# Performance work log

Measured on AMD Instinct MI355X. Metric: run time of the kernel, lower is better.

Reference implementation:

```python
import jax, jax.numpy as jnp
import numpy as np

WH = WW = 8          # window height/width
N_WIN = WH * WW      # tokens per window = 64
DIM = 256
NUM_HEADS = 8
CPB_HIDDEN = 512


def _rel_index():
    # Swin relative position index, shape (N, N), values in [0, (2Wh-1)*(2Ww-1))
    coords = np.stack(np.meshgrid(np.arange(WH), np.arange(WW), indexing='ij'))  # (2,Wh,Ww)
    flat = coords.reshape(2, -1)
    rel = (flat[:, :, None] - flat[:, None, :]).transpose(1, 2, 0)  # (N,N,2)
    rel[..., 0] += WH - 1
    rel[..., 1] += WW - 1
    rel[..., 0] *= 2 * WW - 1
    return rel.sum(-1).astype(np.int32)


def _coords_table():
    # normalized log-spaced continuous relative coordinates, shape (2Wh-1, 2Ww-1, 2)
    h = np.arange(-(WH - 1), WH, dtype=np.float32)
    w = np.arange(-(WW - 1), WW, dtype=np.float32)
    t = np.stack(np.meshgrid(h, w, indexing='ij'), axis=-1)
    t[..., 0] /= WH - 1
    t[..., 1] /= WW - 1
    t *= 8.0
    return (np.sign(t) * np.log2(np.abs(t) + 1.0) / np.log2(8.0)).astype(np.float32)


def setup_inputs() -> dict:
    key = jax.random.key(0)
    ks = jax.random.split(key, 6)
    B_ = 8192  # num_windows * batch
    x = jax.random.normal(ks[0], (B_, N_WIN, DIM), dtype=jnp.float32)
    qkv_weight = jax.random.normal(ks[1], (3 * DIM, DIM), dtype=jnp.float32) * 0.02
    q_bias = jnp.zeros((DIM,), dtype=jnp.float32)
    v_bias = jnp.zeros((DIM,), dtype=jnp.float32)
    logit_scale = jnp.log(10.0) * jnp.ones((NUM_HEADS, 1, 1), dtype=jnp.float32)
    cpb_w1 = jax.random.normal(ks[2], (CPB_HIDDEN, 2), dtype=jnp.float32) * 0.02
    cpb_b1 = jnp.zeros((CPB_HIDDEN,), dtype=jnp.float32)
    cpb_w2 = jax.random.normal(ks[3], (NUM_HEADS, CPB_HIDDEN), dtype=jnp.float32) * 0.02
    proj_w = jax.random.normal(ks[4], (DIM, DIM), dtype=jnp.float32) * 0.02
    proj_b = jnp.zeros((DIM,), dtype=jnp.float32)
    return {
        'x': x, 'qkv_weight': qkv_weight, 'q_bias': q_bias, 'v_bias': v_bias,
        'logit_scale': logit_scale, 'cpb_w1': cpb_w1, 'cpb_b1': cpb_b1,
        'cpb_w2': cpb_w2, 'proj_w': proj_w, 'proj_b': proj_b,
    }


def reference(x, qkv_weight, q_bias, v_bias, logit_scale, cpb_w1, cpb_b1, cpb_w2, proj_w, proj_b):
    B_, N, C = x.shape
    H = NUM_HEADS
    d = C // H
    # qkv projection: k-bias is fixed zero (Swin-V2 convention)
    qkv_b = jnp.concatenate([q_bias, jnp.zeros_like(v_bias), v_bias])
    qkv = x @ qkv_weight.T + qkv_b                       # (B_, N, 3C)
    qkv = qkv.reshape(B_, N, 3, H, d).transpose(2, 0, 3, 1, 4)  # (3, B_, H, N, d)
    q, k, v = qkv[0], qkv[1], qkv[2]
    # cosine attention (F.normalize with eps=1e-12)
    qn = q / jnp.maximum(jnp.linalg.norm(q, axis=-1, keepdims=True), 1e-12)
    kn = k / jnp.maximum(jnp.linalg.norm(k, axis=-1, keepdims=True), 1e-12)
    attn = jnp.einsum('bhnd,bhmd->bhnm', qn, kn)
    scale = jnp.exp(jnp.minimum(logit_scale, jnp.log(100.0)))  # clamp max = log(1/0.01)
    attn = attn * scale                                   # broadcasts (H,1,1)
    # continuous relative position bias via tiny MLP
    table = jnp.asarray(_coords_table())                  # (2Wh-1, 2Ww-1, 2)
    bias_table = jnp.maximum(table @ cpb_w1.T + cpb_b1, 0.0) @ cpb_w2.T  # (.., H)
    bias_table = bias_table.reshape(-1, H)
    idx = jnp.asarray(_rel_index().reshape(-1))
    bias = bias_table[idx].reshape(N, N, H).transpose(2, 0, 1)  # (H, N, N)
    attn = attn + 16.0 * jax.nn.sigmoid(bias)[None]
    attn = jax.nn.softmax(attn, axis=-1)
    out = jnp.einsum('bhnm,bhmd->bhnd', attn, v)          # (B_, H, N, d)
    out = out.transpose(0, 2, 1, 3).reshape(B_, N, C)
    return out @ proj_w.T + proj_b
```

## Files before the change

### kernel.cpp

```cpp
#include <hip/hip_runtime.h>
#include <hip/hip_fp16.h>

typedef _Float16 f16;
typedef _Float16 f16x8 __attribute__((ext_vector_type(8)));
typedef _Float16 f16x4 __attribute__((ext_vector_type(4)));
typedef float f32x4 __attribute__((ext_vector_type(4)));

#define L2E 1.4426950408889634f

#define WQ_OFF   0
#define PW_OFF   393216
#define QB_OFF   524288
#define SC_OFF   527360
#define TBL_OFF  527616
#define BB_OFF   535040


__global__ void prep0(const float* __restrict__ qw, const float* __restrict__ prw,
                      const float* __restrict__ qbias, const float* __restrict__ vbias,
                      const float* __restrict__ ls, char* __restrict__ ws) {
    int t = blockIdx.x * 256 + threadIdx.x;
    f16* wq = (f16*)(ws + WQ_OFF);
    f16* pw = (f16*)(ws + PW_OFF);
    if (t < 196608) wq[t] = (f16)qw[t];
    else            pw[t - 196608] = (f16)prw[t - 196608];
    if (t < 768) {
        float b = t < 256 ? qbias[t] : (t < 512 ? 0.f : vbias[t - 512]);
        ((float*)(ws + QB_OFF))[t] = b;
    }
    if (t < 8) ((float*)(ws + SC_OFF))[t] = expf(fminf(ls[t], 4.6051701859880914f));
}

__device__ __forceinline__ float norm_coord(int u) {
    float v = (float)(u - 7) * (8.0f / 7.0f);
    float s = (v > 0.f) ? 1.f : ((v < 0.f) ? -1.f : 0.f);
    return s * log2f(fabsf(v) + 1.f) * (1.f / 3.f);
}

__global__ void prep1(const float* __restrict__ w1, const float* __restrict__ b1,
                      const float* __restrict__ w2, char* __restrict__ ws) {
    int t = blockIdx.x * 256 + threadIdx.x;
    if (t >= 1800) return;
    int p = t >> 3, h = t & 7;
    float ta = norm_coord(p / 15);
    float tb = norm_coord(p % 15);
    float acc = 0.f;
    for (int j = 0; j < 512; ++j) {
        float hv = fmaf(w1[2 * j], ta, fmaf(w1[2 * j + 1], tb, b1[j]));
        acc = fmaf(fmaxf(hv, 0.f), w2[h * 512 + j], acc);
    }
    ((float*)(ws + TBL_OFF))[p * 8 + h] = acc;
}

__global__ void prep2(char* __restrict__ ws) {
    int t = blockIdx.x * 256 + threadIdx.x;
    int h = t >> 12, i = (t >> 6) & 63, j = t & 63;
    int ri = ((i >> 3) - (j >> 3) + 7) * 15 + ((i & 7) - (j & 7) + 7);
    float bv = ((const float*)(ws + TBL_OFF))[ri * 8 + h];
    float sg = 1.f / (1.f + expf(-bv));
    float sch = ((const float*)(ws + SC_OFF))[h];
    float val = (16.f * sg - sch - 16.f) * L2E + 14.0f;
    int mi = i >> 4, g = (i >> 2) & 3, r = i & 3;
    int nj = j >> 4, c = j & 15;
    int off = h * 4096 + mi * 1024 + nj * 256 + c * 16 + g * 4 + r;
    ((float*)(ws + BB_OFF))[off] = val;
}

#define SWZ(row) (((row) & 7) << 4)
#define LGKM0() asm volatile("s_waitcnt lgkmcnt(0)" ::: "memory")

__global__ __launch_bounds__(256, 2)
void swin_fused(const float* __restrict__ x, const f16* __restrict__ wq,
                const f16* __restrict__ pw, const float* __restrict__ qb,
                const float* __restrict__ sc, const float* __restrict__ bb2,
                const float* __restrict__ pb, float* __restrict__ out) {
    extern __shared__ char lds[];
    const int tid = threadIdx.x;
    const int lane = tid & 63;
    const int w = tid >> 6;
    const int g = lane >> 4;
    const int c = lane & 15;
    const int win = blockIdx.x;
    char* scr = lds + 32768 + w * 5120;

    const float* xw = x + (size_t)win * 16384;
    #pragma unroll
    for (int it = 0; it < 16; ++it) {
        int e4 = tid + it * 256;
        float4 v = ((const float4*)xw)[e4];
        int eidx = e4 * 4;
        int row = eidx >> 8, col = eidx & 255;
        f16x4 h4 = {(f16)v.x, (f16)v.y, (f16)v.z, (f16)v.w};
        int off = ((row << 9) + (col << 1)) ^ SWZ(row);
        *(f16x4*)(lds + off) = h4;
    }
    __syncthreads();

    f16x4 po[4][2];

    for (int hh = 0; hh < 2; ++hh) {
        const int h = w + hh * 4;

        f16x8 vf[2][2];
        {
            f32x4 acc[2][4] = {};
            #pragma unroll 2
            for (int kk = 0; kk < 8; ++kk) {
                int kb = kk * 32 + g * 8;
                f16x8 a[4];
                #pragma unroll
                for (int mi = 0; mi < 4; ++mi) {
                    int row = mi * 16 + c;
                    int off = ((row << 9) + (kb << 1)) ^ SWZ(row);
                    a[mi] = *(const f16x8*)(lds + off);
                }
                #pragma unroll
                for (int t = 0; t < 2; ++t) {
                    f16x8 b = *(const f16x8*)(wq + (size_t)(512 + h * 32 + t * 16 + c) * 256 + kb);
                    #pragma unroll
                    for (int mi = 0; mi < 4; ++mi)
                        acc[t][mi] = __builtin_amdgcn_mfma_f32_16x16x32_f16(a[mi], b, acc[t][mi], 0, 0, 0);
                }
            }
            #pragma unroll
            for (int t = 0; t < 2; ++t) {
                float bias = qb[512 + h * 32 + t * 16 + c];
                #pragma unroll
                for (int mi = 0; mi < 4; ++mi) {
                    f16x4 hv;
                    #pragma unroll
                    for (int r = 0; r < 4; ++r) hv[r] = (f16)(acc[t][mi][r] + bias);
                    int off = (t * 16 + c) * 144 + (mi * 16 + g * 4) * 2;
                    *(f16x4*)(scr + off) = hv;
                }
            }
        }
        LGKM0();
        #pragma unroll
        for (int dt = 0; dt < 2; ++dt)
            #pragma unroll
            for (int kt = 0; kt < 2; ++kt)
                vf[dt][kt] = *(const f16x8*)(scr + (dt * 16 + c) * 144 + kt * 64 + g * 16);
        LGKM0();

        f16x8 qf[4], kf[4];
        {
            f32x4 aq[2][4] = {};
            #pragma unroll 2
            for (int kk = 0; kk < 8; ++kk) {
                int kb = kk * 32 + g * 8;
                f16x8 a[4];
                #pragma unroll
                for (int mi = 0; mi < 4; ++mi) {
                    int row = mi * 16 + c;
                    int off = ((row << 9) + (kb << 1)) ^ SWZ(row);
                    a[mi] = *(const f16x8*)(lds + off);
                }
                #pragma unroll
                for (int t = 0; t < 2; ++t) {
                    f16x8 bq = *(const f16x8*)(wq + (size_t)(h * 32 + t * 16 + c) * 256 + kb);
                    #pragma unroll
                    for (int mi = 0; mi < 4; ++mi)
                        aq[t][mi] = __builtin_amdgcn_mfma_f32_16x16x32_f16(a[mi], bq, aq[t][mi], 0, 0, 0);
                }
            }
            #pragma unroll
            for (int t = 0; t < 2; ++t) {
                float bias = qb[h * 32 + t * 16 + c];
                #pragma unroll
                for (int mi = 0; mi < 4; ++mi)
                    #pragma unroll
                    for (int r = 0; r < 4; ++r) aq[t][mi][r] += bias;
            }
            #pragma unroll
            for (int mi = 0; mi < 4; ++mi) {
                #pragma unroll
                for (int r = 0; r < 4; ++r) {
                    float pq = aq[0][mi][r] * aq[0][mi][r] + aq[1][mi][r] * aq[1][mi][r];
                    pq += __shfl_xor(pq, 1); pq += __shfl_xor(pq, 2);
                    pq += __shfl_xor(pq, 4); pq += __shfl_xor(pq, 8);
                    float rq = __builtin_amdgcn_rsqf(fmaxf(pq, 1e-24f));
                    aq[0][mi][r] *= rq; aq[1][mi][r] *= rq;
                }
            }
            #pragma unroll
            for (int t = 0; t < 2; ++t)
                #pragma unroll
                for (int mi = 0; mi < 4; ++mi)
                    #pragma unroll
                    for (int r = 0; r < 4; ++r) {
                        int off = (mi * 16 + g * 4 + r) * 80 + (t * 16 + c) * 2;
                        *(f16*)(scr + off) = (f16)aq[t][mi][r];
                    }
            LGKM0();
            #pragma unroll
            for (int mi = 0; mi < 4; ++mi)
                qf[mi] = *(const f16x8*)(scr + (mi * 16 + c) * 80 + g * 16);
            LGKM0();
        }
        {
            f32x4 ak[2][4] = {};
            #pragma unroll 2
            for (int kk = 0; kk < 8; ++kk) {
                int kb = kk * 32 + g * 8;
                f16x8 a[4];
                #pragma unroll
                for (int mi = 0; mi < 4; ++mi) {
                    int row = mi * 16 + c;
                    int off = ((row << 9) + (kb << 1)) ^ SWZ(row);
                    a[mi] = *(const f16x8*)(lds + off);
                }
                #pragma unroll
                for (int t = 0; t < 2; ++t) {
                    f16x8 bk = *(const f16x8*)(wq + (size_t)(256 + h * 32 + t * 16 + c) * 256 + kb);
                    #pragma unroll
                    for (int mi = 0; mi < 4; ++mi)
                        ak[t][mi] = __builtin_amdgcn_mfma_f32_16x16x32_f16(a[mi], bk, ak[t][mi], 0, 0, 0);
                }
            }
            #pragma unroll
            for (int mi = 0; mi < 4; ++mi) {
                #pragma unroll
                for (int r = 0; r < 4; ++r) {
                    float pk = ak[0][mi][r] * ak[0][mi][r] + ak[1][mi][r] * ak[1][mi][r];
                    pk += __shfl_xor(pk, 1); pk += __shfl_xor(pk, 2);
                    pk += __shfl_xor(pk, 4); pk += __shfl_xor(pk, 8);
                    float rk = __builtin_amdgcn_rsqf(fmaxf(pk, 1e-24f));
                    ak[0][mi][r] *= rk; ak[1][mi][r] *= rk;
                }
            }
            #pragma unroll
            for (int t = 0; t < 2; ++t)
                #pragma unroll
                for (int mi = 0; mi < 4; ++mi)
                    #pragma unroll
                    for (int r = 0; r < 4; ++r) {
                        int off = (mi * 16 + g * 4 + r) * 80 + (t * 16 + c) * 2;
                        *(f16*)(scr + off) = (f16)ak[t][mi][r];
                    }
            LGKM0();
            #pragma unroll
            for (int nj = 0; nj < 4; ++nj)
                kf[nj] = *(const f16x8*)(scr + (nj * 16 + c) * 80 + g * 16);
            LGKM0();
        }

        if (hh == 1) {
            __syncthreads();
            const int h0 = w;
            #pragma unroll
            for (int mi = 0; mi < 4; ++mi)
                #pragma unroll
                for (int dt = 0; dt < 2; ++dt)
                    #pragma unroll
                    for (int r = 0; r < 4; ++r) {
                        int row = mi * 16 + g * 4 + r;
                        int col = h0 * 32 + dt * 16 + c;
                        int off = ((row << 9) + (col << 1)) ^ SWZ(row);
                        *(f16*)(lds + off) = po[mi][dt][r];
                    }
        }

        const float scl2e = sc[h] * L2E;
        const float* bbw = bb2 + h * 4096;
        f32x4 oo[4][2] = {};
        f32x4 oaux[4] = {};
        f16 onev = (c == 0) ? (f16)1.f : (f16)0.f;
        f16x8 von = {onev, onev, onev, onev, onev, onev, onev, onev};
        #pragma unroll
        for (int nj = 0; nj < 4; ++nj) {
            #pragma unroll
            for (int mi = 0; mi < 4; ++mi) {
                f32x4 z = {};
                f32x4 s = __builtin_amdgcn_mfma_f32_16x16x32_f16(qf[mi], kf[nj], z, 0, 0, 0);
                f32x4 bb4 = *(const f32x4*)(bbw + mi * 1024 + nj * 256 + c * 16 + g * 4);
                #pragma unroll
                for (int r = 0; r < 4; ++r) {
                    float e = exp2f(fmaf(s[r], scl2e, bb4[r]));
                    int off = (mi * 16 + g * 4 + r) * 80 + (((nj & 1) * 16 + c) << 1);
                    *(f16*)(scr + off) = (f16)e;
                }
            }
            if (nj & 1) {
                const int kt = nj >> 1;
                LGKM0();
                f16x8 pa[4];
                #pragma unroll
                for (int mo = 0; mo < 4; ++mo)
                    pa[mo] = *(const f16x8*)(scr + (mo * 16 + c) * 80 + g * 16);
                LGKM0();
                #pragma unroll
                for (int mo = 0; mo < 4; ++mo) {
                    #pragma unroll
                    for (int dt = 0; dt < 2; ++dt)
                        oo[mo][dt] = __builtin_amdgcn_mfma_f32_16x16x32_f16(pa[mo], vf[dt][kt], oo[mo][dt], 0, 0, 0);
                    oaux[mo] = __builtin_amdgcn_mfma_f32_16x16x32_f16(pa[mo], von, oaux[mo], 0, 0, 0);
                }
            }
        }
        #pragma unroll
        for (int mo = 0; mo < 4; ++mo)
            #pragma unroll
            for (int r = 0; r < 4; ++r) {
                float rsum = __shfl(oaux[mo][r], lane & 48);
                float ri = __builtin_amdgcn_rcpf(rsum);
                oo[mo][0][r] *= ri;
                oo[mo][1][r] *= ri;
            }
        if (hh == 0) {
            #pragma unroll
            for (int mi = 0; mi < 4; ++mi)
                #pragma unroll
                for (int dt = 0; dt < 2; ++dt)
                    #pragma unroll
                    for (int r = 0; r < 4; ++r)
                        po[mi][dt][r] = (f16)oo[mi][dt][r];
        } else {
            #pragma unroll
            for (int mi = 0; mi < 4; ++mi)
                #pragma unroll
                for (int dt = 0; dt < 2; ++dt)
                    #pragma unroll
                    for (int r = 0; r < 4; ++r) {
                        int row = mi * 16 + g * 4 + r;
                        int col = h * 32 + dt * 16 + c;
                        int off = ((row << 9) + (col << 1)) ^ SWZ(row);
                        *(f16*)(lds + off) = (f16)oo[mi][dt][r];
                    }
        }
    }
    __syncthreads();

    float pbias[4];
    #pragma unroll
    for (int nt = 0; nt < 4; ++nt) pbias[nt] = pb[w * 64 + nt * 16 + c];
    f32x4 pacc[4][4] = {};
    #pragma unroll 2
    for (int kk = 0; kk < 8; ++kk) {
        int kb = kk * 32 + g * 8;
        f16x8 a[4];
        #pragma unroll
        for (int mi = 0; mi < 4; ++mi) {
            int row = mi * 16 + c;
            int off = ((row << 9) + (kb << 1)) ^ SWZ(row);
            a[mi] = *(const f16x8*)(lds + off);
        }
        #pragma unroll
        for (int nt = 0; nt < 4; ++nt) {
            f16x8 b = *(const f16x8*)(pw + (size_t)(w * 64 + nt * 16 + c) * 256 + kb);
            #pragma unroll
            for (int mi = 0; mi < 4; ++mi)
                pacc[nt][mi] = __builtin_amdgcn_mfma_f32_16x16x32_f16(a[mi], b, pacc[nt][mi], 0, 0, 0);
        }
    }
    __syncthreads();

    #pragma unroll
    for (int p = 0; p < 2; ++p) {
        #pragma unroll
        for (int nt = 0; nt < 4; ++nt)
            #pragma unroll
            for (int m2 = 0; m2 < 2; ++m2) {
                int mi = p * 2 + m2;
                #pragma unroll
                for (int r = 0; r < 4; ++r) {
                    int row = m2 * 16 + g * 4 + r;
                    int col = w * 64 + nt * 16 + c;
                    int off = (row * 1024 + col * 4) ^ ((row & 7) << 4);
                    *(float*)(lds + off) = pacc[nt][mi][r] + pbias[nt];
                }
            }
        __syncthreads();
        float4* out4 = (float4*)(out + (size_t)win * 16384 + p * 8192);
        #pragma unroll
        for (int it = 0; it < 8; ++it) {
            int e4 = it * 256 + tid;
            int off = (e4 * 16) ^ (((e4 >> 6) & 7) << 4);
            out4[e4] = *(const float4*)(lds + off);
        }
        if (p == 0) __syncthreads();
    }
}


extern "C" void kernel_launch(void* const* d_in, const int* in_sizes, int n_in,
                              void* d_out, int out_size, void* d_ws, size_t ws_size,
                              hipStream_t stream) {
    (void)in_sizes; (void)n_in; (void)out_size; (void)ws_size;
    const float* x   = (const float*)d_in[0];
    const float* qw  = (const float*)d_in[1];
    const float* qb_ = (const float*)d_in[2];
    const float* vb_ = (const float*)d_in[3];
    const float* ls  = (const float*)d_in[4];
    const float* w1  = (const float*)d_in[5];
    const float* b1  = (const float*)d_in[6];
    const float* w2  = (const float*)d_in[7];
    const float* prw = (const float*)d_in[8];
    const float* pb  = (const float*)d_in[9];
    float* out = (float*)d_out;
    char* ws = (char*)d_ws;

    prep0<<<1024, 256, 0, stream>>>(qw, prw, qb_, vb_, ls, ws);
    prep1<<<8, 256, 0, stream>>>(w1, b1, w2, ws);
    prep2<<<128, 256, 0, stream>>>(ws);

    (void)hipFuncSetAttribute((const void*)swin_fused,
                              hipFuncAttributeMaxDynamicSharedMemorySize, 53248);
    swin_fused<<<8192, 256, 53248, stream>>>(
        x,
        (const f16*)(ws + WQ_OFF), (const f16*)(ws + PW_OFF),
        (const float*)(ws + QB_OFF), (const float*)(ws + SC_OFF),
        (const float*)(ws + BB_OFF), pb, out);
}
```

Baseline: 772.0 us.

## Raise occupancy to 3 blocks/CU by cutting registers in softmax sum and projection

```diff
diff --git a/kernel.cpp b/kernel.cpp
--- a/kernel.cpp
+++ b/kernel.cpp
@@ -69,7 +69,7 @@
 #define SWZ(row) (((row) & 7) << 4)
 #define LGKM0() asm volatile("s_waitcnt lgkmcnt(0)" ::: "memory")
 
-__global__ __launch_bounds__(256, 2)
+__global__ __launch_bounds__(256, 3)
 void swin_fused(const float* __restrict__ x, const f16* __restrict__ wq,
                 const f16* __restrict__ pw, const float* __restrict__ qb,
                 const float* __restrict__ sc, const float* __restrict__ bb2,
@@ -82,6 +82,7 @@
     const int c = lane & 15;
     const int win = blockIdx.x;
     char* scr = lds + 32768 + w * 5120;
+    char* stg = lds + 32768;
 
     const float* xw = x + (size_t)win * 16384;
     #pragma unroll
@@ -264,9 +265,7 @@
         const float scl2e = sc[h] * L2E;
         const float* bbw = bb2 + h * 4096;
         f32x4 oo[4][2] = {};
-        f32x4 oaux[4] = {};
-        f16 onev = (c == 0) ? (f16)1.f : (f16)0.f;
-        f16x8 von = {onev, onev, onev, onev, onev, onev, onev, onev};
+        f32x4 rs[4] = {};
         #pragma unroll
         for (int nj = 0; nj < 4; ++nj) {
             #pragma unroll
@@ -277,6 +276,7 @@
                 #pragma unroll
                 for (int r = 0; r < 4; ++r) {
                     float e = exp2f(fmaf(s[r], scl2e, bb4[r]));
+                    rs[mi][r] += e;
                     int off = (mi * 16 + g * 4 + r) * 80 + (((nj & 1) * 16 + c) << 1);
                     *(f16*)(scr + off) = (f16)e;
                 }
@@ -290,22 +290,22 @@
                     pa[mo] = *(const f16x8*)(scr + (mo * 16 + c) * 80 + g * 16);
                 LGKM0();
                 #pragma unroll
-                for (int mo = 0; mo < 4; ++mo) {
+                for (int mo = 0; mo < 4; ++mo)
                     #pragma unroll
                     for (int dt = 0; dt < 2; ++dt)
                         oo[mo][dt] = __builtin_amdgcn_mfma_f32_16x16x32_f16(pa[mo], vf[dt][kt], oo[mo][dt], 0, 0, 0);
-                    oaux[mo] = __builtin_amdgcn_mfma_f32_16x16x32_f16(pa[mo], von, oaux[mo], 0, 0, 0);
-                }
             }
         }
         #pragma unroll
-        for (int mo = 0; mo < 4; ++mo)
+        for (int mi = 0; mi < 4; ++mi)
             #pragma unroll
             for (int r = 0; r < 4; ++r) {
-                float rsum = __shfl(oaux[mo][r], lane & 48);
-                float ri = __builtin_amdgcn_rcpf(rsum);
-                oo[mo][0][r] *= ri;
-                oo[mo][1][r] *= ri;
+                float t = rs[mi][r];
+                t += __shfl_xor(t, 1); t += __shfl_xor(t, 2);
+                t += __shfl_xor(t, 4); t += __shfl_xor(t, 8);
+                float ri = __builtin_amdgcn_rcpf(t);
+                oo[mi][0][r] *= ri;
+                oo[mi][1][r] *= ri;
             }
         if (hh == 0) {
             #pragma unroll
@@ -334,51 +334,38 @@
     float pbias[4];
     #pragma unroll
     for (int nt = 0; nt < 4; ++nt) pbias[nt] = pb[w * 64 + nt * 16 + c];
-    f32x4 pacc[4][4] = {};
-    #pragma unroll 2
-    for (int kk = 0; kk < 8; ++kk) {
-        int kb = kk * 32 + g * 8;
-        f16x8 a[4];
-        #pragma unroll
-        for (int mi = 0; mi < 4; ++mi) {
-            int row = mi * 16 + c;
+    for (int cc = 0; cc < 4; ++cc) {
+        f32x4 pacc[4] = {};
+        #pragma unroll 2
+        for (int kk = 0; kk < 8; ++kk) {
+            int kb = kk * 32 + g * 8;
+            int row = cc * 16 + c;
             int off = ((row << 9) + (kb << 1)) ^ SWZ(row);
-            a[mi] = *(const f16x8*)(lds + off);
-        }
-        #pragma unroll
-        for (int nt = 0; nt < 4; ++nt) {
-            f16x8 b = *(const f16x8*)(pw + (size_t)(w * 64 + nt * 16 + c) * 256 + kb);
-            #pragma unroll
-            for (int mi = 0; mi < 4; ++mi)
-                pacc[nt][mi] = __builtin_amdgcn_mfma_f32_16x16x32_f16(a[mi], b, pacc[nt][mi], 0, 0, 0);
-        }
-    }
-    __syncthreads();
-
-    #pragma unroll
-    for (int p = 0; p < 2; ++p) {
+            f16x8 a = *(const f16x8*)(lds + off);
+            #pragma unroll
+            for (int nt = 0; nt < 4; ++nt) {
+                f16x8 b = *(const f16x8*)(pw + (size_t)(w * 64 + nt * 16 + c) * 256 + kb);
+                pacc[nt] = __builtin_amdgcn_mfma_f32_16x16x32_f16(a, b, pacc[nt], 0, 0, 0);
+            }
+        }
+        __syncthreads();
         #pragma unroll
         for (int nt = 0; nt < 4; ++nt)
             #pragma unroll
-            for (int m2 = 0; m2 < 2; ++m2) {
-                int mi = p * 2 + m2;
-                #pragma unroll
-                for (int r = 0; r < 4; ++r) {
-                    int row = m2 * 16 + g * 4 + r;
-                    int col = w * 64 + nt * 16 + c;
-                    int off = (row * 1024 + col * 4) ^ ((row & 7) << 4);
-                    *(float*)(lds + off) = pacc[nt][mi][r] + pbias[nt];
-                }
+            for (int r = 0; r < 4; ++r) {
+                int row = g * 4 + r;
+                int col = w * 64 + nt * 16 + c;
+                int off = (row * 1024 + col * 4) ^ ((row & 7) << 4);
+                *(float*)(stg + off) = pacc[nt][r] + pbias[nt];
             }
         __syncthreads();
-        float4* out4 = (float4*)(out + (size_t)win * 16384 + p * 8192);
+        float4* out4 = (float4*)(out + (size_t)win * 16384 + cc * 4096);
         #pragma unroll
-        for (int it = 0; it < 8; ++it) {
+        for (int it = 0; it < 4; ++it) {
             int e4 = it * 256 + tid;
             int off = (e4 * 16) ^ (((e4 >> 6) & 7) << 4);
-            out4[e4] = *(const float4*)(lds + off);
-        }
-        if (p == 0) __syncthreads();
+            out4[e4] = *(const float4*)(stg + off);
+        }
     }
 }
 
```

After: 1.260 ms. +63.2%, slower.

## Replace LDS round-trips for Q/K/V fragments with register shuffles and transposed MFMAs

Applied to the files above, without the earlier changes.

```diff
diff --git a/kernel.cpp b/kernel.cpp
--- a/kernel.cpp
+++ b/kernel.cpp
@@ -64,6 +64,27 @@
     int nj = j >> 4, c = j & 15;
     int off = h * 4096 + mi * 1024 + nj * 256 + c * 16 + g * 4 + r;
     ((float*)(ws + BB_OFF))[off] = val;
+}
+
+__device__ __forceinline__ void packh4(f32x4 v, unsigned &lo, unsigned &hi) {
+    union { f16x4 h; unsigned u[2]; } t;
+    t.h[0] = (f16)v[0]; t.h[1] = (f16)v[1]; t.h[2] = (f16)v[2]; t.h[3] = (f16)v[3];
+    lo = t.u[0]; hi = t.u[1];
+}
+__device__ __forceinline__ f16x8 xchg4(unsigned p0l, unsigned p0h,
+                                       unsigned p1l, unsigned p1h,
+                                       int g, int c) {
+    int sLo = ((g & 1) << 5) + c;
+    int sHi = sLo + 16;
+    unsigned a0 = (unsigned)__shfl((int)p0l, sLo), a1 = (unsigned)__shfl((int)p0h, sLo);
+    unsigned b0 = (unsigned)__shfl((int)p1l, sLo), b1 = (unsigned)__shfl((int)p1h, sLo);
+    unsigned c0 = (unsigned)__shfl((int)p0l, sHi), c1 = (unsigned)__shfl((int)p0h, sHi);
+    unsigned d0 = (unsigned)__shfl((int)p1l, sHi), d1 = (unsigned)__shfl((int)p1h, sHi);
+    bool up = g >= 2;
+    union { f16x8 h; unsigned u[4]; } r;
+    r.u[0] = up ? b0 : a0; r.u[1] = up ? b1 : a1;
+    r.u[2] = up ? d0 : c0; r.u[3] = up ? d1 : c1;
+    return r.h;
 }
 
 #define SWZ(row) (((row) & 7) << 4)
@@ -100,10 +121,10 @@
 
     for (int hh = 0; hh < 2; ++hh) {
         const int h = w + hh * 4;
-
-        f16x8 vf[2][2];
+        f16x8 vf[2][2], qf[4], kf[4];
+
         {
-            f32x4 acc[2][4] = {};
+            f32x4 av[2][4] = {};
             #pragma unroll 2
             for (int kk = 0; kk < 8; ++kk) {
                 int kb = kk * 32 + g * 8;
@@ -119,31 +140,31 @@
                     f16x8 b = *(const f16x8*)(wq + (size_t)(512 + h * 32 + t * 16 + c) * 256 + kb);
                     #pragma unroll
                     for (int mi = 0; mi < 4; ++mi)
-                        acc[t][mi] = __builtin_amdgcn_mfma_f32_16x16x32_f16(a[mi], b, acc[t][mi], 0, 0, 0);
+                        av[t][mi] = __builtin_amdgcn_mfma_f32_16x16x32_f16(a[mi], b, av[t][mi], 0, 0, 0);
                 }
             }
             #pragma unroll
             for (int t = 0; t < 2; ++t) {
                 float bias = qb[512 + h * 32 + t * 16 + c];
                 #pragma unroll
-                for (int mi = 0; mi < 4; ++mi) {
-                    f16x4 hv;
-                    #pragma unroll
-                    for (int r = 0; r < 4; ++r) hv[r] = (f16)(acc[t][mi][r] + bias);
-                    int off = (t * 16 + c) * 144 + (mi * 16 + g * 4) * 2;
-                    *(f16x4*)(scr + off) = hv;
-                }
-            }
-        }
-        LGKM0();
-        #pragma unroll
-        for (int dt = 0; dt < 2; ++dt)
-            #pragma unroll
-            for (int kt = 0; kt < 2; ++kt)
-                vf[dt][kt] = *(const f16x8*)(scr + (dt * 16 + c) * 144 + kt * 64 + g * 16);
-        LGKM0();
-
-        f16x8 qf[4], kf[4];
+                for (int mi = 0; mi < 4; ++mi)
+                    #pragma unroll
+                    for (int r = 0; r < 4; ++r) av[t][mi][r] += bias;
+            }
+            unsigned pv[2][4][2];
+            #pragma unroll
+            for (int t = 0; t < 2; ++t)
+                #pragma unroll
+                for (int mi = 0; mi < 4; ++mi)
+                    packh4(av[t][mi], pv[t][mi][0], pv[t][mi][1]);
+            #pragma unroll
+            for (int dt = 0; dt < 2; ++dt)
+                #pragma unroll
+                for (int kt = 0; kt < 2; ++kt)
+                    vf[dt][kt] = xchg4(pv[dt][2 * kt][0], pv[dt][2 * kt][1],
+                                       pv[dt][2 * kt + 1][0], pv[dt][2 * kt + 1][1], g, c);
+        }
+
         {
             f32x4 aq[2][4] = {};
             #pragma unroll 2
@@ -151,52 +172,48 @@
                 int kb = kk * 32 + g * 8;
                 f16x8 a[4];
                 #pragma unroll
-                for (int mi = 0; mi < 4; ++mi) {
-                    int row = mi * 16 + c;
+                for (int nt = 0; nt < 4; ++nt) {
+                    int row = nt * 16 + c;
                     int off = ((row << 9) + (kb << 1)) ^ SWZ(row);
-                    a[mi] = *(const f16x8*)(lds + off);
-                }
-                #pragma unroll
-                for (int t = 0; t < 2; ++t) {
-                    f16x8 bq = *(const f16x8*)(wq + (size_t)(h * 32 + t * 16 + c) * 256 + kb);
-                    #pragma unroll
-                    for (int mi = 0; mi < 4; ++mi)
-                        aq[t][mi] = __builtin_amdgcn_mfma_f32_16x16x32_f16(a[mi], bq, aq[t][mi], 0, 0, 0);
-                }
-            }
-            #pragma unroll
-            for (int t = 0; t < 2; ++t) {
-                float bias = qb[h * 32 + t * 16 + c];
-                #pragma unroll
-                for (int mi = 0; mi < 4; ++mi)
-                    #pragma unroll
-                    for (int r = 0; r < 4; ++r) aq[t][mi][r] += bias;
-            }
-            #pragma unroll
-            for (int mi = 0; mi < 4; ++mi) {
-                #pragma unroll
-                for (int r = 0; r < 4; ++r) {
-                    float pq = aq[0][mi][r] * aq[0][mi][r] + aq[1][mi][r] * aq[1][mi][r];
-                    pq += __shfl_xor(pq, 1); pq += __shfl_xor(pq, 2);
-                    pq += __shfl_xor(pq, 4); pq += __shfl_xor(pq, 8);
-                    float rq = __builtin_amdgcn_rsqf(fmaxf(pq, 1e-24f));
-                    aq[0][mi][r] *= rq; aq[1][mi][r] *= rq;
-                }
-            }
-            #pragma unroll
-            for (int t = 0; t < 2; ++t)
-                #pragma unroll
-                for (int mi = 0; mi < 4; ++mi)
-                    #pragma unroll
-                    for (int r = 0; r < 4; ++r) {
-                        int off = (mi * 16 + g * 4 + r) * 80 + (t * 16 + c) * 2;
-                        *(f16*)(scr + off) = (f16)aq[t][mi][r];
-                    }
-            LGKM0();
-            #pragma unroll
-            for (int mi = 0; mi < 4; ++mi)
-                qf[mi] = *(const f16x8*)(scr + (mi * 16 + c) * 80 + g * 16);
-            LGKM0();
+                    a[nt] = *(const f16x8*)(lds + off);
+                }
+                #pragma unroll
+                for (int mt = 0; mt < 2; ++mt) {
+                    f16x8 bq = *(const f16x8*)(wq + (size_t)(h * 32 + mt * 16 + c) * 256 + kb);
+                    #pragma unroll
+                    for (int nt = 0; nt < 4; ++nt)
+                        aq[mt][nt] = __builtin_amdgcn_mfma_f32_16x16x32_f16(bq, a[nt], aq[mt][nt], 0, 0, 0);
+                }
+            }
+            f32x4 qb4[2];
+            #pragma unroll
+            for (int mt = 0; mt < 2; ++mt)
+                qb4[mt] = *(const f32x4*)(qb + h * 32 + mt * 16 + g * 4);
+            #pragma unroll
+            for (int mt = 0; mt < 2; ++mt)
+                #pragma unroll
+                for (int nt = 0; nt < 4; ++nt)
+                    aq[mt][nt] += qb4[mt];
+            #pragma unroll
+            for (int nt = 0; nt < 4; ++nt) {
+                float pq = 0.f;
+                #pragma unroll
+                for (int mt = 0; mt < 2; ++mt)
+                    #pragma unroll
+                    for (int r = 0; r < 4; ++r) pq = fmaf(aq[mt][nt][r], aq[mt][nt][r], pq);
+                pq += __shfl_xor(pq, 16);
+                pq += __shfl_xor(pq, 32);
+                float rq = __builtin_amdgcn_rsqf(fmaxf(pq, 1e-24f));
+                #pragma unroll
+                for (int mt = 0; mt < 2; ++mt) aq[mt][nt] *= rq;
+            }
+            #pragma unroll
+            for (int nt = 0; nt < 4; ++nt) {
+                unsigned q0l, q0h, q1l, q1h;
+                packh4(aq[0][nt], q0l, q0h);
+                packh4(aq[1][nt], q1l, q1h);
+                qf[nt] = xchg4(q0l, q0h, q1l, q1h, g, c);
+            }
         }
         {
             f32x4 ak[2][4] = {};
@@ -205,44 +222,39 @@
                 int kb = kk * 32 + g * 8;
                 f16x8 a[4];
                 #pragma unroll
-                for (int mi = 0; mi < 4; ++mi) {
-                    int row = mi * 16 + c;
+                for (int nt = 0; nt < 4; ++nt) {
+                    int row = nt * 16 + c;
                     int off = ((row << 9) + (kb << 1)) ^ SWZ(row);
-                    a[mi] = *(const f16x8*)(lds + off);
-                }
-                #pragma unroll
-                for (int t = 0; t < 2; ++t) {
-                    f16x8 bk = *(const f16x8*)(wq + (size_t)(256 + h * 32 + t * 16 + c) * 256 + kb);
-                    #pragma unroll
-                    for (int mi = 0; mi < 4; ++mi)
-                        ak[t][mi] = __builtin_amdgcn_mfma_f32_16x16x32_f16(a[mi], bk, ak[t][mi], 0, 0, 0);
-                }
-            }
-            #pragma unroll
-            for (int mi = 0; mi < 4; ++mi) {
-                #pragma unroll
-                for (int r = 0; r < 4; ++r) {
-                    float pk = ak[0][mi][r] * ak[0][mi][r] + ak[1][mi][r] * ak[1][mi][r];
-                    pk += __shfl_xor(pk, 1); pk += __shfl_xor(pk, 2);
-                    pk += __shfl_xor(pk, 4); pk += __shfl_xor(pk, 8);
-                    float rk = __builtin_amdgcn_rsqf(fmaxf(pk, 1e-24f));
-                    ak[0][mi][r] *= rk; ak[1][mi][r] *= rk;
-                }
-            }
-            #pragma unroll
-            for (int t = 0; t < 2; ++t)
-                #pragma unroll
-                for (int mi = 0; mi < 4; ++mi)
-                    #pragma unroll
-                    for (int r = 0; r < 4; ++r) {
-                        int off = (mi * 16 + g * 4 + r) * 80 + (t * 16 + c) * 2;
-                        *(f16*)(scr + off) = (f16)ak[t][mi][r];
-                    }
-            LGKM0();
-            #pragma unroll
-            for (int nj = 0; nj < 4; ++nj)
-                kf[nj] = *(const f16x8*)(scr + (nj * 16 + c) * 80 + g * 16);
-            LGKM0();
+                    a[nt] = *(const f16x8*)(lds + off);
+                }
+                #pragma unroll
+                for (int mt = 0; mt < 2; ++mt) {
+                    f16x8 bk = *(const f16x8*)(wq + (size_t)(256 + h * 32 + mt * 16 + c) * 256 + kb);
+                    #pragma unroll
+                    for (int nt = 0; nt < 4; ++nt)
+                        ak[mt][nt] = __builtin_amdgcn_mfma_f32_16x16x32_f16(bk, a[nt], ak[mt][nt], 0, 0, 0);
+                }
+            }
+            #pragma unroll
+            for (int nt = 0; nt < 4; ++nt) {
+                float pk = 0.f;
+                #pragma unroll
+                for (int mt = 0; mt < 2; ++mt)
+                    #pragma unroll
+                    for (int r = 0; r < 4; ++r) pk = fmaf(ak[mt][nt][r], ak[mt][nt][r], pk);
+                pk += __shfl_xor(pk, 16);
+                pk += __shfl_xor(pk, 32);
+                float rk = __builtin_amdgcn_rsqf(fmaxf(pk, 1e-24f));
+                #pragma unroll
+                for (int mt = 0; mt < 2; ++mt) ak[mt][nt] *= rk;
+            }
+            #pragma unroll
+            for (int nt = 0; nt < 4; ++nt) {
+                unsigned k0l, k0h, k1l, k1h;
+                packh4(ak[0][nt], k0l, k0h);
+                packh4(ak[1][nt], k1l, k1h);
+                kf[nt] = xchg4(k0l, k0h, k1l, k1h, g, c);
+            }
         }
 
         if (hh == 1) {
@@ -264,9 +276,7 @@
         const float scl2e = sc[h] * L2E;
         const float* bbw = bb2 + h * 4096;
         f32x4 oo[4][2] = {};
-        f32x4 oaux[4] = {};
-        f16 onev = (c == 0) ? (f16)1.f : (f16)0.f;
-        f16x8 von = {onev, onev, onev, onev, onev, onev, onev, onev};
+        f32x4 rs[4] = {};
         #pragma unroll
         for (int nj = 0; nj < 4; ++nj) {
             #pragma unroll
@@ -277,6 +287,7 @@
                 #pragma unroll
                 for (int r = 0; r < 4; ++r) {
                     float e = exp2f(fmaf(s[r], scl2e, bb4[r]));
+                    rs[mi][r] += e;
                     int off = (mi * 16 + g * 4 + r) * 80 + (((nj & 1) * 16 + c) << 1);
                     *(f16*)(scr + off) = (f16)e;
                 }
@@ -290,22 +301,22 @@
                     pa[mo] = *(const f16x8*)(scr + (mo * 16 + c) * 80 + g * 16);
                 LGKM0();
                 #pragma unroll
-                for (int mo = 0; mo < 4; ++mo) {
+                for (int mo = 0; mo < 4; ++mo)
                     #pragma unroll
                     for (int dt = 0; dt < 2; ++dt)
                         oo[mo][dt] = __builtin_amdgcn_mfma_f32_16x16x32_f16(pa[mo], vf[dt][kt], oo[mo][dt], 0, 0, 0);
-                    oaux[mo] = __builtin_amdgcn_mfma_f32_16x16x32_f16(pa[mo], von, oaux[mo], 0, 0, 0);
-                }
-            }
-        }
-        #pragma unroll
-        for (int mo = 0; mo < 4; ++mo)
+            }
+        }
+        #pragma unroll
+        for (int mi = 0; mi < 4; ++mi)
             #pragma unroll
             for (int r = 0; r < 4; ++r) {
-                float rsum = __shfl(oaux[mo][r], lane & 48);
-                float ri = __builtin_amdgcn_rcpf(rsum);
-                oo[mo][0][r] *= ri;
-                oo[mo][1][r] *= ri;
+                float t = rs[mi][r];
+                t += __shfl_xor(t, 1); t += __shfl_xor(t, 2);
+                t += __shfl_xor(t, 4); t += __shfl_xor(t, 8);
+                float ri = __builtin_amdgcn_rcpf(t);
+                oo[mi][0][r] *= ri;
+                oo[mi][1][r] *= ri;
             }
         if (hh == 0) {
             #pragma unroll
```

Result: slower. 984.9 us (+27.6%).

## Make fused Swin kernel persistent with register prefetch of next window

Applied to the files above, without the earlier changes.

```diff
diff --git a/kernel.cpp b/kernel.cpp
--- a/kernel.cpp
+++ b/kernel.cpp
@@ -80,305 +80,330 @@
     const int w = tid >> 6;
     const int g = lane >> 4;
     const int c = lane & 15;
-    const int win = blockIdx.x;
     char* scr = lds + 32768 + w * 5120;
 
-    const float* xw = x + (size_t)win * 16384;
-    #pragma unroll
+    float4 pf[16];
+
     for (int it = 0; it < 16; ++it) {
-        int e4 = tid + it * 256;
-        float4 v = ((const float4*)xw)[e4];
-        int eidx = e4 * 4;
-        int row = eidx >> 8, col = eidx & 255;
-        f16x4 h4 = {(f16)v.x, (f16)v.y, (f16)v.z, (f16)v.w};
-        int off = ((row << 9) + (col << 1)) ^ SWZ(row);
-        *(f16x4*)(lds + off) = h4;
-    }
-    __syncthreads();
-
-    f16x4 po[4][2];
-
-    for (int hh = 0; hh < 2; ++hh) {
-        const int h = w + hh * 4;
-
-        f16x8 vf[2][2];
-        {
-            f32x4 acc[2][4] = {};
-            #pragma unroll 2
-            for (int kk = 0; kk < 8; ++kk) {
-                int kb = kk * 32 + g * 8;
-                f16x8 a[4];
+        const int win = blockIdx.x + it * 512;
+
+        if (it == 0) {
+            const float* xw = x + (size_t)win * 16384;
+            #pragma unroll
+            for (int q = 0; q < 16; ++q) {
+                int e4 = tid + q * 256;
+                float4 v = ((const float4*)xw)[e4];
+                int eidx = e4 * 4;
+                int row = eidx >> 8, col = eidx & 255;
+                f16x4 h4 = {(f16)v.x, (f16)v.y, (f16)v.z, (f16)v.w};
+                int off = ((row << 9) + (col << 1)) ^ SWZ(row);
+                *(f16x4*)(lds + off) = h4;
+            }
+        } else {
+            #pragma unroll
+            for (int q = 0; q < 16; ++q) {
+                int e4 = tid + q * 256;
+                int eidx = e4 * 4;
+                int row = eidx >> 8, col = eidx & 255;
+                f16x4 h4 = {(f16)pf[q].x, (f16)pf[q].y, (f16)pf[q].z, (f16)pf[q].w};
+                int off = ((row << 9) + (col << 1)) ^ SWZ(row);
+                *(f16x4*)(lds + off) = h4;
+            }
+        }
+        __syncthreads();
+
+        f16x4 po[4][2];
+
+        for (int hh = 0; hh < 2; ++hh) {
+            const int h = w + hh * 4;
+
+            f16x8 vf[2][2];
+            {
+                f32x4 acc[2][4] = {};
+                #pragma unroll 2
+                for (int kk = 0; kk < 8; ++kk) {
+                    int kb = kk * 32 + g * 8;
+                    f16x8 a[4];
+                    #pragma unroll
+                    for (int mi = 0; mi < 4; ++mi) {
+                        int row = mi * 16 + c;
+                        int off = ((row << 9) + (kb << 1)) ^ SWZ(row);
+                        a[mi] = *(const f16x8*)(lds + off);
+                    }
+                    #pragma unroll
+                    for (int t = 0; t < 2; ++t) {
+                        f16x8 b = *(const f16x8*)(wq + (size_t)(512 + h * 32 + t * 16 + c) * 256 + kb);
+                        #pragma unroll
+                        for (int mi = 0; mi < 4; ++mi)
+                            acc[t][mi] = __builtin_amdgcn_mfma_f32_16x16x32_f16(a[mi], b, acc[t][mi], 0, 0, 0);
+                    }
+                }
+                #pragma unroll
+                for (int t = 0; t < 2; ++t) {
+                    float bias = qb[512 + h * 32 + t * 16 + c];
+                    #pragma unroll
+                    for (int mi = 0; mi < 4; ++mi) {
+                        f16x4 hv;
+                        #pragma unroll
+                        for (int r = 0; r < 4; ++r) hv[r] = (f16)(acc[t][mi][r] + bias);
+                        int off = (t * 16 + c) * 144 + (mi * 16 + g * 4) * 2;
+                        *(f16x4*)(scr + off) = hv;
+                    }
+                }
+            }
+            LGKM0();
+            #pragma unroll
+            for (int dt = 0; dt < 2; ++dt)
+                #pragma unroll
+                for (int kt = 0; kt < 2; ++kt)
+                    vf[dt][kt] = *(const f16x8*)(scr + (dt * 16 + c) * 144 + kt * 64 + g * 16);
+            LGKM0();
+
+            f16x8 qf[4], kf[4];
+            {
+                f32x4 aq[2][4] = {};
+                #pragma unroll 2
+                for (int kk = 0; kk < 8; ++kk) {
+                    int kb = kk * 32 + g * 8;
+                    f16x8 a[4];
+                    #pragma unroll
+                    for (int mi = 0; mi < 4; ++mi) {
+                        int row = mi * 16 + c;
+                        int off = ((row << 9) + (kb << 1)) ^ SWZ(row);
+                        a[mi] = *(const f16x8*)(lds + off);
+                    }
+                    #pragma unroll
+                    for (int t = 0; t < 2; ++t) {
+                        f16x8 bq = *(const f16x8*)(wq + (size_t)(h * 32 + t * 16 + c) * 256 + kb);
+                        #pragma unroll
+                        for (int mi = 0; mi < 4; ++mi)
+                            aq[t][mi] = __builtin_amdgcn_mfma_f32_16x16x32_f16(a[mi], bq, aq[t][mi], 0, 0, 0);
+                    }
+                }
+                #pragma unroll
+                for (int t = 0; t < 2; ++t) {
+                    float bias = qb[h * 32 + t * 16 + c];
+                    #pragma unroll
+                    for (int mi = 0; mi < 4; ++mi)
+                        #pragma unroll
+                        for (int r = 0; r < 4; ++r) aq[t][mi][r] += bias;
+                }
                 #pragma unroll
                 for (int mi = 0; mi < 4; ++mi) {
-                    int row = mi * 16 + c;
-                    int off = ((row << 9) + (kb << 1)) ^ SWZ(row);
-                    a[mi] = *(const f16x8*)(lds + off);
-                }
-                #pragma unroll
-                for (int t = 0; t < 2; ++t) {
-                    f16x8 b = *(const f16x8*)(wq + (size_t)(512 + h * 32 + t * 16 + c) * 256 + kb);
+                    #pragma unroll
+                    for (int r = 0; r < 4; ++r) {
+                        float pq = aq[0][mi][r] * aq[0][mi][r] + aq[1][mi][r] * aq[1][mi][r];
+                        pq += __shfl_xor(pq, 1); pq += __shfl_xor(pq, 2);
+                        pq += __shfl_xor(pq, 4); pq += __shfl_xor(pq, 8);
+                        float rq = __builtin_amdgcn_rsqf(fmaxf(pq, 1e-24f));
+                        aq[0][mi][r] *= rq; aq[1][mi][r] *= rq;
+                    }
+                }
+                #pragma unroll
+                for (int t = 0; t < 2; ++t)
                     #pragma unroll
                     for (int mi = 0; mi < 4; ++mi)
-                        acc[t][mi] = __builtin_amdgcn_mfma_f32_16x16x32_f16(a[mi], b, acc[t][mi], 0, 0, 0);
-                }
-            }
-            #pragma unroll
-            for (int t = 0; t < 2; ++t) {
-                float bias = qb[512 + h * 32 + t * 16 + c];
+                        #pragma unroll
+                        for (int r = 0; r < 4; ++r) {
+                            int off = (mi * 16 + g * 4 + r) * 80 + (t * 16 + c) * 2;
+                            *(f16*)(scr + off) = (f16)aq[t][mi][r];
+                        }
+                LGKM0();
+                #pragma unroll
+                for (int mi = 0; mi < 4; ++mi)
+                    qf[mi] = *(const f16x8*)(scr + (mi * 16 + c) * 80 + g * 16);
+                LGKM0();
+            }
+            {
+                f32x4 ak[2][4] = {};
+                #pragma unroll 2
+                for (int kk = 0; kk < 8; ++kk) {
+                    int kb = kk * 32 + g * 8;
+                    f16x8 a[4];
+                    #pragma unroll
+                    for (int mi = 0; mi < 4; ++mi) {
+                        int row = mi * 16 + c;
+                        int off = ((row << 9) + (kb << 1)) ^ SWZ(row);
+                        a[mi] = *(const f16x8*)(lds + off);
+                    }
+                    #pragma unroll
+                    for (int t = 0; t < 2; ++t) {
+                        f16x8 bk = *(const f16x8*)(wq + (size_t)(256 + h * 32 + t * 16 + c) * 256 + kb);
+                        #pragma unroll
+                        for (int mi = 0; mi < 4; ++mi)
+                            ak[t][mi] = __builtin_amdgcn_mfma_f32_16x16x32_f16(a[mi], bk, ak[t][mi], 0, 0, 0);
+                    }
+                }
                 #pragma unroll
                 for (int mi = 0; mi < 4; ++mi) {
-                    f16x4 hv;
-                    #pragma unroll
-                    for (int r = 0; r < 4; ++r) hv[r] = (f16)(acc[t][mi][r] + bias);
-                    int off = (t * 16 + c) * 144 + (mi * 16 + g * 4) * 2;
-                    *(f16x4*)(scr + off) = hv;
-                }
+                    #pragma unroll
+                    for (int r = 0; r < 4; ++r) {
+                        float pk = ak[0][mi][r] * ak[0][mi][r] + ak[1][mi][r] * ak[1][mi][r];
+                        pk += __shfl_xor(pk, 1); pk += __shfl_xor(pk, 2);
+                        pk += __shfl_xor(pk, 4); pk += __shfl_xor(pk, 8);
+                        float rk = __builtin_amdgcn_rsqf(fmaxf(pk, 1e-24f));
+                        ak[0][mi][r] *= rk; ak[1][mi][r] *= rk;
+                    }
+                }
+                #pragma unroll
+                for (int t = 0; t < 2; ++t)
+                    #pragma unroll
+                    for (int mi = 0; mi < 4; ++mi)
+                        #pragma unroll
+                        for (int r = 0; r < 4; ++r) {
+                            int off = (mi * 16 + g * 4 + r) * 80 + (t * 16 + c) * 2;
+                            *(f16*)(scr + off) = (f16)ak[t][mi][r];
+                        }
+                LGKM0();
+                #pragma unroll
+                for (int nj = 0; nj < 4; ++nj)
+                    kf[nj] = *(const f16x8*)(scr + (nj * 16 + c) * 80 + g * 16);
+                LGKM0();
+            }
+
+            if (hh == 1) {
+                __syncthreads();
+                const int h0 = w;
+                #pragma unroll
+                for (int mi = 0; mi < 4; ++mi)
+                    #pragma unroll
+                    for (int dt = 0; dt < 2; ++dt)
+                        #pragma unroll
+                        for (int r = 0; r < 4; ++r) {
+                            int row = mi * 16 + g * 4 + r;
+                            int col = h0 * 32 + dt * 16 + c;
+                            int off = ((row << 9) + (col << 1)) ^ SWZ(row);
+                            *(f16*)(lds + off) = po[mi][dt][r];
+                        }
+            }
+
+            const float scl2e = sc[h] * L2E;
+            const float* bbw = bb2 + h * 4096;
+            f32x4 oo[4][2] = {};
+            f32x4 oaux[4] = {};
+            f16 onev = (c == 0) ? (f16)1.f : (f16)0.f;
+            f16x8 von = {onev, onev, onev, onev, onev, onev, onev, onev};
+            #pragma unroll
+            for (int nj = 0; nj < 4; ++nj) {
+                #pragma unroll
+                for (int mi = 0; mi < 4; ++mi) {
+                    f32x4 z = {};
+                    f32x4 s = __builtin_amdgcn_mfma_f32_16x16x32_f16(qf[mi], kf[nj], z, 0, 0, 0);
+                    f32x4 bb4 = *(const f32x4*)(bbw + mi * 1024 + nj * 256 + c * 16 + g * 4);
+                    #pragma unroll
+                    for (int r = 0; r < 4; ++r) {
+                        float e = exp2f(fmaf(s[r], scl2e, bb4[r]));
+                        int off = (mi * 16 + g * 4 + r) * 80 + (((nj & 1) * 16 + c) << 1);
+                        *(f16*)(scr + off) = (f16)e;
+                    }
+                }
+                if (nj & 1) {
+                    const int kt = nj >> 1;
+                    LGKM0();
+                    f16x8 pa[4];
+                    #pragma unroll
+                    for (int mo = 0; mo < 4; ++mo)
+                        pa[mo] = *(const f16x8*)(scr + (mo * 16 + c) * 80 + g * 16);
+                    LGKM0();
+                    #pragma unroll
+                    for (int mo = 0; mo < 4; ++mo) {
+                        #pragma unroll
+                        for (int dt = 0; dt < 2; ++dt)
+                            oo[mo][dt] = __builtin_amdgcn_mfma_f32_16x16x32_f16(pa[mo], vf[dt][kt], oo[mo][dt], 0, 0, 0);
+                        oaux[mo] = __builtin_amdgcn_mfma_f32_16x16x32_f16(pa[mo], von, oaux[mo], 0, 0, 0);
+                    }
+                }
+            }
+            #pragma unroll
+            for (int mo = 0; mo < 4; ++mo)
+                #pragma unroll
+                for (int r = 0; r < 4; ++r) {
+                    float rsum = __shfl(oaux[mo][r], lane & 48);
+                    float ri = __builtin_amdgcn_rcpf(rsum);
+                    oo[mo][0][r] *= ri;
+                    oo[mo][1][r] *= ri;
+                }
+            if (hh == 0) {
+                #pragma unroll
+                for (int mi = 0; mi < 4; ++mi)
+                    #pragma unroll
+                    for (int dt = 0; dt < 2; ++dt)
+                        #pragma unroll
+                        for (int r = 0; r < 4; ++r)
+                            po[mi][dt][r] = (f16)oo[mi][dt][r];
+            } else {
+                #pragma unroll
+                for (int mi = 0; mi < 4; ++mi)
+                    #pragma unroll
+                    for (int dt = 0; dt < 2; ++dt)
+                        #pragma unroll
+                        for (int r = 0; r < 4; ++r) {
+                            int row = mi * 16 + g * 4 + r;
+                            int col = h * 32 + dt * 16 + c;
+                            int off = ((row << 9) + (col << 1)) ^ SWZ(row);
+                            *(f16*)(lds + off) = (f16)oo[mi][dt][r];
+                        }
             }
         }
-        LGKM0();
+        __syncthreads();
+
+        if (it < 15) {
+            const float* xn = x + (size_t)(win + 512) * 16384;
+            #pragma unroll
+            for (int q = 0; q < 16; ++q)
+                pf[q] = ((const float4*)xn)[tid + q * 256];
+        }
+
+        float pbias[4];
         #pragma unroll
-        for (int dt = 0; dt < 2; ++dt)
-            #pragma unroll
-            for (int kt = 0; kt < 2; ++kt)
-                vf[dt][kt] = *(const f16x8*)(scr + (dt * 16 + c) * 144 + kt * 64 + g * 16);
-        LGKM0();
-
-        f16x8 qf[4], kf[4];
-        {
-            f32x4 aq[2][4] = {};
-            #pragma unroll 2
-            for (int kk = 0; kk < 8; ++kk) {
-                int kb = kk * 32 + g * 8;
-                f16x8 a[4];
-                #pragma unroll
-                for (int mi = 0; mi < 4; ++mi) {
-                    int row = mi * 16 + c;
-                    int off = ((row << 9) + (kb << 1)) ^ SWZ(row);
-                    a[mi] = *(const f16x8*)(lds + off);
-                }
-                #pragma unroll
-                for (int t = 0; t < 2; ++t) {
-                    f16x8 bq = *(const f16x8*)(wq + (size_t)(h * 32 + t * 16 + c) * 256 + kb);
-                    #pragma unroll
-                    for (int mi = 0; mi < 4; ++mi)
-                        aq[t][mi] = __builtin_amdgcn_mfma_f32_16x16x32_f16(a[mi], bq, aq[t][mi], 0, 0, 0);
-                }
-            }
-            #pragma unroll
-            for (int t = 0; t < 2; ++t) {
-                float bias = qb[h * 32 + t * 16 + c];
+        for (int nt = 0; nt < 4; ++nt) pbias[nt] = pb[w * 64 + nt * 16 + c];
+        f32x4 pacc[4][4] = {};
+        #pragma unroll 2
+        for (int kk = 0; kk < 8; ++kk) {
+            int kb = kk * 32 + g * 8;
+            f16x8 a[4];
+            #pragma unroll
+            for (int mi = 0; mi < 4; ++mi) {
+                int row = mi * 16 + c;
+                int off = ((row << 9) + (kb << 1)) ^ SWZ(row);
+                a[mi] = *(const f16x8*)(lds + off);
+            }
+            #pragma unroll
+            for (int nt = 0; nt < 4; ++nt) {
+                f16x8 b = *(const f16x8*)(pw + (size_t)(w * 64 + nt * 16 + c) * 256 + kb);
                 #pragma unroll
                 for (int mi = 0; mi < 4; ++mi)
-                    #pragma unroll
-                    for (int r = 0; r < 4; ++r) aq[t][mi][r] += bias;
-            }
-            #pragma unroll
-            for (int mi = 0; mi < 4; ++mi) {
-                #pragma unroll
-                for (int r = 0; r < 4; ++r) {
-                    float pq = aq[0][mi][r] * aq[0][mi][r] + aq[1][mi][r] * aq[1][mi][r];
-                    pq += __shfl_xor(pq, 1); pq += __shfl_xor(pq, 2);
-                    pq += __shfl_xor(pq, 4); pq += __shfl_xor(pq, 8);
-                    float rq = __builtin_amdgcn_rsqf(fmaxf(pq, 1e-24f));
-                    aq[0][mi][r] *= rq; aq[1][mi][r] *= rq;
-                }
-            }
-            #pragma unroll
-            for (int t = 0; t < 2; ++t)
-                #pragma unroll
-                for (int mi = 0; mi < 4; ++mi)
+                    pacc[nt][mi] = __builtin_amdgcn_mfma_f32_16x16x32_f16(a[mi], b, pacc[nt][mi], 0, 0, 0);
+            }
+        }
+        __syncthreads();
+
+        #pragma unroll
+        for (int p = 0; p < 2; ++p) {
+            #pragma unroll
+            for (int nt = 0; nt < 4; ++nt)
+                #pragma unroll
+                for (int m2 = 0; m2 < 2; ++m2) {
+                    int mi = p * 2 + m2;
                     #pragma unroll
                     for (int r = 0; r < 4; ++r) {
-                        int off = (mi * 16 + g * 4 + r) * 80 + (t * 16 + c) * 2;
-                        *(f16*)(scr + off) = (f16)aq[t][mi][r];
-                    }
-            LGKM0();
-            #pragma unroll
-            for (int mi = 0; mi < 4; ++mi)
-                qf[mi] = *(const f16x8*)(scr + (mi * 16 + c) * 80 + g * 16);
-            LGKM0();
+                        int row = m2 * 16 + g * 4 + r;
+                        int col = w * 64 + nt * 16 + c;
+                        int off = (row * 1024 + col * 4) ^ ((row & 7) << 4);
+                        *(float*)(lds + off) = pacc[nt][mi][r] + pbias[nt];
+                    }
+                }
+            __syncthreads();
+            float4* out4 = (float4*)(out + (size_t)win * 16384 + p * 8192);
+            #pragma unroll
+            for (int q = 0; q < 8; ++q) {
+                int e4 = q * 256 + tid;
+                int off = (e4 * 16) ^ (((e4 >> 6) & 7) << 4);
+                out4[e4] = *(const float4*)(lds + off);
+            }
+            if (p == 0) __syncthreads();
         }
-        {
-            f32x4 ak[2][4] = {};
-            #pragma unroll 2
-            for (int kk = 0; kk < 8; ++kk) {
-                int kb = kk * 32 + g * 8;
-                f16x8 a[4];
-                #pragma unroll
-                for (int mi = 0; mi < 4; ++mi) {
-                    int row = mi * 16 + c;
-                    int off = ((row << 9) + (kb << 1)) ^ SWZ(row);
-                    a[mi] = *(const f16x8*)(lds + off);
-                }
-                #pragma unroll
-                for (int t = 0; t < 2; ++t) {
-                    f16x8 bk = *(const f16x8*)(wq + (size_t)(256 + h * 32 + t * 16 + c) * 256 + kb);
-                    #pragma unroll
-                    for (int mi = 0; mi < 4; ++mi)
-                        ak[t][mi] = __builtin_amdgcn_mfma_f32_16x16x32_f16(a[mi], bk, ak[t][mi], 0, 0, 0);
-                }
-            }
-            #pragma unroll
-            for (int mi = 0; mi < 4; ++mi) {
-                #pragma unroll
-                for (int r = 0; r < 4; ++r) {
-                    float pk = ak[0][mi][r] * ak[0][mi][r] + ak[1][mi][r] * ak[1][mi][r];
-                    pk += __shfl_xor(pk, 1); pk += __shfl_xor(pk, 2);
-                    pk += __shfl_xor(pk, 4); pk += __shfl_xor(pk, 8);
-                    float rk = __builtin_amdgcn_rsqf(fmaxf(pk, 1e-24f));
-                    ak[0][mi][r] *= rk; ak[1][mi][r] *= rk;
-                }
-            }
-            #pragma unroll
-            for (int t = 0; t < 2; ++t)
-                #pragma unroll
-                for (int mi = 0; mi < 4; ++mi)
-                    #pragma unroll
-                    for (int r = 0; r < 4; ++r) {
-                        int off = (mi * 16 + g * 4 + r) * 80 + (t * 16 + c) * 2;
-                        *(f16*)(scr + off) = (f16)ak[t][mi][r];
-                    }
-            LGKM0();
-            #pragma unroll
-            for (int nj = 0; nj < 4; ++nj)
-                kf[nj] = *(const f16x8*)(scr + (nj * 16 + c) * 80 + g * 16);
-            LGKM0();
-        }
-
-        if (hh == 1) {
-            __syncthreads();
-            const int h0 = w;
-            #pragma unroll
-            for (int mi = 0; mi < 4; ++mi)
-                #pragma unroll
-                for (int dt = 0; dt < 2; ++dt)
-                    #pragma unroll
-                    for (int r = 0; r < 4; ++r) {
-                        int row = mi * 16 + g * 4 + r;
-                        int col = h0 * 32 + dt * 16 + c;
-                        int off = ((row << 9) + (col << 1)) ^ SWZ(row);
-                        *(f16*)(lds + off) = po[mi][dt][r];
-                    }
-        }
-
-        const float scl2e = sc[h] * L2E;
-        const float* bbw = bb2 + h * 4096;
-        f32x4 oo[4][2] = {};
-        f32x4 oaux[4] = {};
-        f16 onev = (c == 0) ? (f16)1.f : (f16)0.f;
-        f16x8 von = {onev, onev, onev, onev, onev, onev, onev, onev};
-        #pragma unroll
-        for (int nj = 0; nj < 4; ++nj) {
-            #pragma unroll
-            for (int mi = 0; mi < 4; ++mi) {
-                f32x4 z = {};
-                f32x4 s = __builtin_amdgcn_mfma_f32_16x16x32_f16(qf[mi], kf[nj], z, 0, 0, 0);
-                f32x4 bb4 = *(const f32x4*)(bbw + mi * 1024 + nj * 256 + c * 16 + g * 4);
-                #pragma unroll
-                for (int r = 0; r < 4; ++r) {
-                    float e = exp2f(fmaf(s[r], scl2e, bb4[r]));
-                    int off = (mi * 16 + g * 4 + r) * 80 + (((nj & 1) * 16 + c) << 1);
-                    *(f16*)(scr + off) = (f16)e;
-                }
-            }
-            if (nj & 1) {
-                const int kt = nj >> 1;
-                LGKM0();
-                f16x8 pa[4];
-                #pragma unroll
-                for (int mo = 0; mo < 4; ++mo)
-                    pa[mo] = *(const f16x8*)(scr + (mo * 16 + c) * 80 + g * 16);
-                LGKM0();
-                #pragma unroll
-                for (int mo = 0; mo < 4; ++mo) {
-                    #pragma unroll
-                    for (int dt = 0; dt < 2; ++dt)
-                        oo[mo][dt] = __builtin_amdgcn_mfma_f32_16x16x32_f16(pa[mo], vf[dt][kt], oo[mo][dt], 0, 0, 0);
-                    oaux[mo] = __builtin_amdgcn_mfma_f32_16x16x32_f16(pa[mo], von, oaux[mo], 0, 0, 0);
-                }
-            }
-        }
-        #pragma unroll
-        for (int mo = 0; mo < 4; ++mo)
-            #pragma unroll
-            for (int r = 0; r < 4; ++r) {
-                float rsum = __shfl(oaux[mo][r], lane & 48);
-                float ri = __builtin_amdgcn_rcpf(rsum);
-                oo[mo][0][r] *= ri;
-                oo[mo][1][r] *= ri;
-            }
-        if (hh == 0) {
-            #pragma unroll
-            for (int mi = 0; mi < 4; ++mi)
-                #pragma unroll
-                for (int dt = 0; dt < 2; ++dt)
-                    #pragma unroll
-                    for (int r = 0; r < 4; ++r)
-                        po[mi][dt][r] = (f16)oo[mi][dt][r];
-        } else {
-            #pragma unroll
-            for (int mi = 0; mi < 4; ++mi)
-                #pragma unroll
-                for (int dt = 0; dt < 2; ++dt)
-                    #pragma unroll
-                    for (int r = 0; r < 4; ++r) {
-                        int row = mi * 16 + g * 4 + r;
-                        int col = h * 32 + dt * 16 + c;
-                        int off = ((row << 9) + (col << 1)) ^ SWZ(row);
-                        *(f16*)(lds + off) = (f16)oo[mi][dt][r];
-                    }
-        }
-    }
-    __syncthreads();
-
-    float pbias[4];
-    #pragma unroll
-    for (int nt = 0; nt < 4; ++nt) pbias[nt] = pb[w * 64 + nt * 16 + c];
-    f32x4 pacc[4][4] = {};
-    #pragma unroll 2
-    for (int kk = 0; kk < 8; ++kk) {
-        int kb = kk * 32 + g * 8;
-        f16x8 a[4];
-        #pragma unroll
-        for (int mi = 0; mi < 4; ++mi) {
-            int row = mi * 16 + c;
-            int off = ((row << 9) + (kb << 1)) ^ SWZ(row);
-            a[mi] = *(const f16x8*)(lds + off);
-        }
-        #pragma unroll
-        for (int nt = 0; nt < 4; ++nt) {
-            f16x8 b = *(const f16x8*)(pw + (size_t)(w * 64 + nt * 16 + c) * 256 + kb);
-            #pragma unroll
-            for (int mi = 0; mi < 4; ++mi)
-                pacc[nt][mi] = __builtin_amdgcn_mfma_f32_16x16x32_f16(a[mi], b, pacc[nt][mi], 0, 0, 0);
-        }
-    }
-    __syncthreads();
-
-    #pragma unroll
-    for (int p = 0; p < 2; ++p) {
-        #pragma unroll
-        for (int nt = 0; nt < 4; ++nt)
-            #pragma unroll
-            for (int m2 = 0; m2 < 2; ++m2) {
-                int mi = p * 2 + m2;
-                #pragma unroll
-                for (int r = 0; r < 4; ++r) {
-                    int row = m2 * 16 + g * 4 + r;
-                    int col = w * 64 + nt * 16 + c;
-                    int off = (row * 1024 + col * 4) ^ ((row & 7) << 4);
-                    *(float*)(lds + off) = pacc[nt][mi][r] + pbias[nt];
-                }
-            }
         __syncthreads();
-        float4* out4 = (float4*)(out + (size_t)win * 16384 + p * 8192);
-        #pragma unroll
-        for (int it = 0; it < 8; ++it) {
-            int e4 = it * 256 + tid;
-            int off = (e4 * 16) ^ (((e4 >> 6) & 7) << 4);
-            out4[e4] = *(const float4*)(lds + off);
-        }
-        if (p == 0) __syncthreads();
     }
 }
 
@@ -406,7 +431,7 @@
 
     (void)hipFuncSetAttribute((const void*)swin_fused,
                               hipFuncAttributeMaxDynamicSharedMemorySize, 53248);
-    swin_fused<<<8192, 256, 53248, stream>>>(
+    swin_fused<<<512, 256, 53248, stream>>>(
         x,
         (const f16*)(ws + WQ_OFF), (const f16*)(ws + PW_OFF),
         (const float*)(ws + QB_OFF), (const float*)(ws + SC_OFF),
```

Result: slower. 1.213 ms (+57.2%).
